# Optimization experiments

Measured on AMD Instinct MI355X. Metric: run time of the kernel, lower is better.

Reference implementation:

```python
import jax, jax.numpy as jnp
import numpy as np


def setup_inputs() -> dict:
    key = jax.random.key(0)
    B, T, V, H, C = 128, 256, 128, 512, 128  # batch, seq_length, input_dim, num_hidden, num_classes
    ks = jax.random.split(key, 10)

    def xavier(k, shape):
        fan_in, fan_out = shape
        lim = jnp.sqrt(6.0 / (fan_in + fan_out)).astype(jnp.float32)
        return jax.random.uniform(k, shape, jnp.float32, -lim, lim)

    inp = {
        'x': jax.random.randint(ks[0], (B, T), 0, V, dtype=jnp.int32),
        'W_xg': xavier(ks[1], (V, H)), 'W_hg': xavier(ks[2], (H, H)),
        'W_xi': xavier(ks[3], (V, H)), 'W_hi': xavier(ks[4], (H, H)),
        'W_xf': xavier(ks[5], (V, H)), 'W_hf': xavier(ks[6], (H, H)),
        'W_xo': xavier(ks[7], (V, H)), 'W_ho': xavier(ks[8], (H, H)),
        'W_hp': xavier(ks[9], (H, C)),
        'b_g': jnp.zeros((H,), jnp.float32), 'b_i': jnp.zeros((H,), jnp.float32),
        'b_f': jnp.zeros((H,), jnp.float32), 'b_o': jnp.zeros((H,), jnp.float32),
        'b_p': jnp.zeros((C,), jnp.float32),
    }
    return inp


def reference(x, W_xg, W_hg, W_xi, W_hi, W_xf, W_hf, W_xo, W_ho, W_hp,
              b_g, b_i, b_f, b_o, b_p):
    B, T = x.shape
    H = W_hg.shape[0]
    # one-hot(x_t) @ W_x* == row-gather W_x*[x_t]; same math, no dense one-hot.
    xs = x[:, : T - 1].T  # [T-1, B] token ids; loop runs seq_length-1 steps

    def step(carry, idx):
        h, c = carry
        g = jnp.tanh(W_xg[idx] + h @ W_hg + b_g)
        i = jax.nn.sigmoid(W_xi[idx] + h @ W_hi + b_i)
        f = jax.nn.sigmoid(W_xf[idx] + h @ W_hf + b_f)
        o = jax.nn.sigmoid(W_xo[idx] + h @ W_ho + b_o)
        c = g * i + c * f
        h = jnp.tanh(c) * o
        return (h, c), None

    h0 = jnp.zeros((B, H), jnp.float32)
    c0 = jnp.zeros((B, H), jnp.float32)
    (h, _), _ = jax.lax.scan(step, (h0, c0), xs)
    return h @ W_hp + b_p
```

## Files before the change

kernel.cpp:

```cpp
#include <hip/hip_runtime.h>


typedef __attribute__((ext_vector_type(8))) short short8;
typedef __attribute__((ext_vector_type(4))) float f32x4;
typedef __attribute__((ext_vector_type(4))) unsigned int u32x4;
typedef __attribute__((ext_vector_type(8))) unsigned int u32x8;
typedef __attribute__((ext_vector_type(16))) unsigned int u32x16;

#define NGROUPS 8
#define WGS_PER_GROUP 32
#define HDIM 512
#define TT 256
#define NSTEPS 255
#define CDIM 128
#define PGQ 4096
#define TAGB_OFF 1024

__device__ unsigned long long g_hbuf[4 * NGROUPS * PGQ];
__device__ unsigned int g_sync[TAGB_OFF + NGROUPS * WGS_PER_GROUP * 16];

static __device__ __forceinline__ unsigned short f32_to_bf16(float f) {
  unsigned int u = __builtin_bit_cast(unsigned int, f);
  u += 0x7fffu + ((u >> 16) & 1u);
  return (unsigned short)(u >> 16);
}
static __device__ __forceinline__ float bf16_to_f32(unsigned short s) {
  unsigned int u = ((unsigned int)s) << 16;
  return __builtin_bit_cast(float, u);
}
static __device__ __forceinline__ float fast_sigmoid(float v) {
  return __builtin_amdgcn_rcpf(1.0f + __expf(-v));
}
static __device__ __forceinline__ float fast_tanh(float v) {
  return 1.0f - 2.0f * __builtin_amdgcn_rcpf(1.0f + __expf(2.0f * v));
}
static __device__ __forceinline__ const unsigned int* sgpr_ptr(const unsigned int* p) {
  const unsigned long long u = (unsigned long long)p;
  const unsigned int lo = __builtin_amdgcn_readfirstlane((unsigned int)u);
  const unsigned int hi = __builtin_amdgcn_readfirstlane((unsigned int)(u >> 32));
  return (const unsigned int*)(((unsigned long long)hi << 32) | (unsigned long long)lo);
}

static __device__ __forceinline__ unsigned int poll_min8(const unsigned int* p) {
  u32x8 A;
  asm volatile("s_dcache_inv\n\t"
               "s_load_dwordx8 %0, %1, 0x0\n\t"
               "s_waitcnt lgkmcnt(0)"
               : "=&s"(A) : "s"(p) : "memory");
  unsigned int m = A[0];
#pragma unroll
  for (int i = 1; i < 8; ++i) m = (A[i] < m) ? A[i] : m;
  return m;
}
static __device__ __forceinline__ unsigned int poll_min32(const unsigned int* p) {
  u32x16 A, B;
  asm volatile("s_dcache_inv\n\t"
               "s_load_dwordx16 %0, %1, 0x0\n\t"
               "s_waitcnt lgkmcnt(0)"
               : "=&s"(A) : "s"(p) : "memory");
  unsigned int m = A[0];
#pragma unroll
  for (int i = 1; i < 16; ++i) m = (A[i] < m) ? A[i] : m;
  asm volatile("s_load_dwordx16 %0, %1, 0x40\n\t"
               "s_waitcnt lgkmcnt(0)"
               : "=&s"(B) : "s"(p) : "memory");
#pragma unroll
  for (int i = 0; i < 16; ++i) m = (B[i] < m) ? B[i] : m;
  return m;
}

static __device__ __forceinline__ void wait_prod8(const unsigned int* tag8,
                                                  const unsigned int* tagBlane,
                                                  unsigned int tgt) {
  for (int spins = 0; spins < 4096; ++spins) {
    if (poll_min8(tag8) >= tgt) return;
  }
  for (;;) {
    const unsigned int v = __hip_atomic_load(tagBlane, __ATOMIC_RELAXED,
                                             __HIP_MEMORY_SCOPE_AGENT);
    if (__all((int)(v >= tgt))) return;
    __builtin_amdgcn_s_sleep(1);
  }
}
static __device__ __forceinline__ void wait_group32(const unsigned int* tagA,
                                                    const unsigned int* tagBlane,
                                                    unsigned int tgt) {
  for (int spins = 0; spins < 4096; ++spins) {
    if (poll_min32(tagA) >= tgt) return;
  }
  for (;;) {
    const unsigned int v = __hip_atomic_load(tagBlane, __ATOMIC_RELAXED,
                                             __HIP_MEMORY_SCOPE_AGENT);
    if (__all((int)(v >= tgt))) return;
    __builtin_amdgcn_s_sleep(1);
  }
}

__global__ __launch_bounds__(256, 1) void lstm_persistent(
    const int* __restrict__ x,
    const float* __restrict__ Wxg, const float* __restrict__ Whg,
    const float* __restrict__ Wxi, const float* __restrict__ Whi,
    const float* __restrict__ Wxf, const float* __restrict__ Whf,
    const float* __restrict__ Wxo, const float* __restrict__ Who,
    const float* __restrict__ Whp,
    const float* __restrict__ bg, const float* __restrict__ bi,
    const float* __restrict__ bf, const float* __restrict__ bo,
    const float* __restrict__ bp,
    float* __restrict__ out)
{
  const int bid = blockIdx.x;
  const int g = bid & 7;
  const int w = bid >> 3;
  const int tid = threadIdx.x;
  const int wave = tid >> 6;
  const int lane = tid & 63;
  const int lane15 = lane & 15;
  const int lanehi = lane >> 4;

  __shared__ float part[2][4][4][16][16];
  __shared__ int lds_x[16][TT];
  __shared__ unsigned int lds_ctr;

  if (tid == 0) lds_ctr = 0u;
  for (int i = tid; i < 16 * TT; i += 256)
    ((int*)lds_x)[i] = x[g * 16 * TT + i];

  const float* Whs[4] = {Whg, Whi, Whf, Who};
  const int bcol = (w << 4) + lane15;
  short8 wf[4][4][2];
#pragma unroll
  for (int gate = 0; gate < 4; ++gate) {
    const float* Wh = Whs[gate];
#pragma unroll
    for (int ksl = 0; ksl < 4; ++ksl) {
      const int ksg = (wave << 2) + ksl;
      short8 s0, s1;
#pragma unroll
      for (int e = 0; e < 8; ++e) {
        float v = Wh[(ksg * 32 + lanehi * 8 + e) * HDIM + bcol];
        unsigned short a = f32_to_bf16(v);
        unsigned short b = f32_to_bf16(v - bf16_to_f32(a));
        s0[e] = (short)a; s1[e] = (short)b;
      }
      wf[gate][ksl][0] = s0; wf[gate][ksl][1] = s1;
    }
  }
  __syncthreads();

  const int brow = tid >> 4;
  const int jl = tid & 15;
  const int j = (w << 4) + jl;
  const float bgv = bg[j], biv = bi[j], bfv = bf[j], bov = bo[j];
  const int pidx = ((j >> 5) << 8) + ((((j >> 3) & 3) << 4) + brow) * 4 + ((j & 7) >> 1);

  const unsigned int* tagA = sgpr_ptr(g_sync + (g << 5));
  const unsigned int* tag8 = sgpr_ptr(g_sync + (g << 5) + (wave << 3));
  const unsigned int* tagBlane =
      g_sync + TAGB_OFF + ((unsigned)(g * 32 + (lane & 31)) << 4);
  unsigned int* myA = g_sync + (g << 5) + w;
  unsigned int* myB = g_sync + TAGB_OFF + ((unsigned)(g * 32 + w) << 4);

  float creg = 0.0f;

  for (int t = 0; t < NSTEPS; ++t) {
    const int idx = lds_x[brow][t];
    const float xgv = Wxg[idx * HDIM + j];
    const float xiv = Wxi[idx * HDIM + j];
    const float xfv = Wxf[idx * HDIM + j];
    const float xov = Wxo[idx * HDIM + j];

    f32x4 acc[4] = {{0.f,0.f,0.f,0.f},{0.f,0.f,0.f,0.f},
                    {0.f,0.f,0.f,0.f},{0.f,0.f,0.f,0.f}};
    if (t > 0) {
      wait_prod8(tag8, tagBlane, (unsigned int)t);
      const unsigned long long* srcq =
          g_hbuf + ((size_t)((t & 3) * NGROUPS + g)) * PGQ;
      unsigned long long q[16];
#pragma unroll
      for (int ksl = 0; ksl < 4; ++ksl) {
        const int base = ((wave << 2) + ksl) * 256 + (lane << 2);
#pragma unroll
        for (int u = 0; u < 4; ++u)
          q[ksl * 4 + u] = srcq[base + u];
      }
#pragma unroll
      for (int ksl = 0; ksl < 4; ++ksl) {
        u32x4 lo, hi;
#pragma unroll
        for (int u = 0; u < 4; ++u) {
          lo[u] = (unsigned int)q[ksl * 4 + u];
          hi[u] = (unsigned int)(q[ksl * 4 + u] >> 32);
        }
        const short8 a0 = __builtin_bit_cast(short8, lo);
        const short8 a1 = __builtin_bit_cast(short8, hi);
#pragma unroll
        for (int gate = 0; gate < 4; ++gate) {
          acc[gate] = __builtin_amdgcn_mfma_f32_16x16x32_bf16(a0, wf[gate][ksl][0], acc[gate], 0, 0, 0);
          acc[gate] = __builtin_amdgcn_mfma_f32_16x16x32_bf16(a0, wf[gate][ksl][1], acc[gate], 0, 0, 0);
          acc[gate] = __builtin_amdgcn_mfma_f32_16x16x32_bf16(a1, wf[gate][ksl][0], acc[gate], 0, 0, 0);
        }
      }
    }
    {
      const int crow = lanehi << 2;
      const int pb = t & 1;
#pragma unroll
      for (int gate = 0; gate < 4; ++gate)
#pragma unroll
        for (int r = 0; r < 4; ++r)
          part[pb][wave][gate][crow + r][lane15] = acc[gate][r];
    }
    __syncthreads();

    const int pb = t & 1;
    const float pg = part[pb][0][0][brow][jl] + part[pb][1][0][brow][jl] +
                     part[pb][2][0][brow][jl] + part[pb][3][0][brow][jl] + xgv + bgv;
    const float pi = part[pb][0][1][brow][jl] + part[pb][1][1][brow][jl] +
                     part[pb][2][1][brow][jl] + part[pb][3][1][brow][jl] + xiv + biv;
    const float pf = part[pb][0][2][brow][jl] + part[pb][1][2][brow][jl] +
                     part[pb][2][2][brow][jl] + part[pb][3][2][brow][jl] + xfv + bfv;
    const float po = part[pb][0][3][brow][jl] + part[pb][1][3][brow][jl] +
                     part[pb][2][3][brow][jl] + part[pb][3][3][brow][jl] + xov + bov;
    const float gv = fast_tanh(pg);
    const float iv = fast_sigmoid(pi);
    const float fv = fast_sigmoid(pf);
    const float ov = fast_sigmoid(po);
    creg = gv * iv + creg * fv;
    const float hv = fast_tanh(creg) * ov;

    const unsigned short h0 = f32_to_bf16(hv);
    const unsigned short h1 = f32_to_bf16(hv - bf16_to_f32(h0));
    const unsigned int pa = (unsigned int)h0 | ((unsigned int)h1 << 16);
    const unsigned int na = (unsigned int)__shfl_xor((int)pa, 1);
    if (!(jl & 1)) {
      unsigned long long* dstq =
          g_hbuf + ((size_t)(((t + 1) & 3) * NGROUPS + g)) * PGQ;
      const unsigned int w0 = (pa & 0xffffu) | ((na & 0xffffu) << 16);
      const unsigned int w1 = (pa >> 16) | (na & 0xffff0000u);
      dstq[pidx] = (unsigned long long)w0 | ((unsigned long long)w1 << 32);
    }
    asm volatile("s_waitcnt vmcnt(0)" ::: "memory");
    if (lane == 0) {
      const unsigned int old = atomicAdd(&lds_ctr, 1u);
      if ((old & 3u) == 3u) {
        __hip_atomic_store(myA, (unsigned int)(t + 1), __ATOMIC_RELAXED,
                           __HIP_MEMORY_SCOPE_WORKGROUP);
        __hip_atomic_store(myB, (unsigned int)(t + 1), __ATOMIC_RELAXED,
                           __HIP_MEMORY_SCOPE_AGENT);
      }
    }
  }

  wait_group32(tagA, tagBlane, (unsigned int)NSTEPS);
  __syncthreads();
  {
    const unsigned long long* srcq =
        g_hbuf + ((size_t)((NSTEPS & 3) * NGROUPS + g)) * PGQ;
    const int bq = tid >> 4;
    const int q15 = tid & 15;
    const int cloc = q15 >> 2;
    const int ksl2 = q15 & 3;
    const int cc = (w << 2) + cloc;
    float sum = 0.0f;
    for (int k = ksl2 * 128; k < ksl2 * 128 + 128; k += 2) {
      const int pk = ((k >> 5) << 8) + ((((k >> 3) & 3) << 4) + bq) * 4 + ((k & 7) >> 1);
      const unsigned long long qv = srcq[pk];
      const unsigned int w0 = (unsigned int)qv;
      const unsigned int w1 = (unsigned int)(qv >> 32);
      const float hk0 = bf16_to_f32((unsigned short)(w0 & 0xffffu)) +
                        bf16_to_f32((unsigned short)(w1 & 0xffffu));
      const float hk1 = bf16_to_f32((unsigned short)(w0 >> 16)) +
                        bf16_to_f32((unsigned short)(w1 >> 16));
      sum += hk0 * Whp[k * CDIM + cc] + hk1 * Whp[(k + 1) * CDIM + cc];
    }
    float* gb = &part[0][0][0][0][0];
    gb[tid] = sum;
    __syncthreads();
    if (ksl2 == 0) {
      const float res = gb[tid] + gb[tid + 1] + gb[tid + 2] + gb[tid + 3] + bp[cc];
      out[(g * 16 + bq) * CDIM + cc] = res;
    }
  }
}

extern "C" void kernel_launch(void* const* d_in, const int* in_sizes, int n_in,
                              void* d_out, int out_size, void* d_ws, size_t ws_size,
                              hipStream_t stream) {
  (void)in_sizes; (void)n_in; (void)out_size; (void)d_ws; (void)ws_size;
  const int* x = (const int*)d_in[0];
  const float* Wxg = (const float*)d_in[1];
  const float* Whg = (const float*)d_in[2];
  const float* Wxi = (const float*)d_in[3];
  const float* Whi = (const float*)d_in[4];
  const float* Wxf = (const float*)d_in[5];
  const float* Whf = (const float*)d_in[6];
  const float* Wxo = (const float*)d_in[7];
  const float* Who = (const float*)d_in[8];
  const float* Whp = (const float*)d_in[9];
  const float* bg = (const float*)d_in[10];
  const float* bi = (const float*)d_in[11];
  const float* bf = (const float*)d_in[12];
  const float* bo = (const float*)d_in[13];
  const float* bp = (const float*)d_in[14];
  float* out = (float*)d_out;

  void* sync_dev = nullptr;
  hipGetSymbolAddress(&sync_dev, HIP_SYMBOL(g_sync));
  hipMemsetAsync(sync_dev, 0,
                 sizeof(unsigned int) * (TAGB_OFF + NGROUPS * WGS_PER_GROUP * 16),
                 stream);

  lstm_persistent<<<dim3(256), dim3(256), 0, stream>>>(
      x, Wxg, Whg, Wxi, Whi, Wxf, Whf, Wxo, Who, Whp,
      bg, bi, bf, bo, bp, out);
}
```

Measured before the change: 417.4 us.

## Split hidden-state buffer into hi/lo planes and vectorize partial-sum LDS layout

The global h exchange buffer changes from interleaved 64-bit hi/lo pairs to two separate 32-bit planes, so each lane loads each MFMA operand with one 16-byte vector load instead of four 64-bit loads followed by unpacking. The MFMA chain is split across two accumulator sets to shorten the dependency chain. The LDS partial-sum layout becomes gate-innermost, so each thread does one float4 store per row and four float4 loads in the reduction. The cost is two scalar stores per producer instead of one 64-bit store.

Measured after the change: 418.1 us. About the same (+0.2%).

```diff
diff --git a/kernel.cpp b/kernel.cpp
--- a/kernel.cpp
+++ b/kernel.cpp
@@ -3,7 +3,6 @@
 
 typedef __attribute__((ext_vector_type(8))) short short8;
 typedef __attribute__((ext_vector_type(4))) float f32x4;
-typedef __attribute__((ext_vector_type(4))) unsigned int u32x4;
 typedef __attribute__((ext_vector_type(8))) unsigned int u32x8;
 typedef __attribute__((ext_vector_type(16))) unsigned int u32x16;
 
@@ -13,10 +12,11 @@
 #define TT 256
 #define NSTEPS 255
 #define CDIM 128
-#define PGQ 4096
+#define PGW 8192
+#define PLANE_W 4096
 #define TAGB_OFF 1024
 
-__device__ unsigned long long g_hbuf[4 * NGROUPS * PGQ];
+__device__ unsigned int g_hbuf[4 * NGROUPS * PGW];
 __device__ unsigned int g_sync[TAGB_OFF + NGROUPS * WGS_PER_GROUP * 16];
 
 static __device__ __forceinline__ unsigned short f32_to_bf16(float f) {
@@ -117,7 +117,7 @@
   const int lane15 = lane & 15;
   const int lanehi = lane >> 4;
 
-  __shared__ float part[2][4][4][16][16];
+  __shared__ __align__(16) float part[2][4][16][16][4];
   __shared__ int lds_x[16][TT];
   __shared__ unsigned int lds_ctr;
 
@@ -151,7 +151,8 @@
   const int jl = tid & 15;
   const int j = (w << 4) + jl;
   const float bgv = bg[j], biv = bi[j], bfv = bf[j], bov = bo[j];
-  const int pidx = ((j >> 5) << 8) + ((((j >> 3) & 3) << 4) + brow) * 4 + ((j & 7) >> 1);
+  const int woff32 = ((j >> 5) << 8) + ((((j >> 3) & 3) << 4) + brow) * 4 + ((j & 7) >> 1);
+  const unsigned int voff = ((unsigned)wave << 12) + ((unsigned)lane << 4);
 
   const unsigned int* tagA = sgpr_ptr(g_sync + (g << 5));
   const unsigned int* tag8 = sgpr_ptr(g_sync + (g << 5) + (wave << 3));
@@ -169,35 +170,36 @@
     const float xfv = Wxf[idx * HDIM + j];
     const float xov = Wxo[idx * HDIM + j];
 
-    f32x4 acc[4] = {{0.f,0.f,0.f,0.f},{0.f,0.f,0.f,0.f},
-                    {0.f,0.f,0.f,0.f},{0.f,0.f,0.f,0.f}};
+    f32x4 accA[4] = {{0.f,0.f,0.f,0.f},{0.f,0.f,0.f,0.f},
+                     {0.f,0.f,0.f,0.f},{0.f,0.f,0.f,0.f}};
+    f32x4 accB[4] = {{0.f,0.f,0.f,0.f},{0.f,0.f,0.f,0.f},
+                     {0.f,0.f,0.f,0.f},{0.f,0.f,0.f,0.f}};
     if (t > 0) {
       wait_prod8(tag8, tagBlane, (unsigned int)t);
-      const unsigned long long* srcq =
-          g_hbuf + ((size_t)((t & 3) * NGROUPS + g)) * PGQ;
-      unsigned long long q[16];
+      const char* p0 = (const char*)(g_hbuf +
+          ((size_t)((t & 3) * NGROUPS + g)) * PGW) + voff;
+      short8 a0[4], a1[4];
 #pragma unroll
       for (int ksl = 0; ksl < 4; ++ksl) {
-        const int base = ((wave << 2) + ksl) * 256 + (lane << 2);
-#pragma unroll
-        for (int u = 0; u < 4; ++u)
-          q[ksl * 4 + u] = srcq[base + u];
-      }
-#pragma unroll
-      for (int ksl = 0; ksl < 4; ++ksl) {
-        u32x4 lo, hi;
-#pragma unroll
-        for (int u = 0; u < 4; ++u) {
-          lo[u] = (unsigned int)q[ksl * 4 + u];
-          hi[u] = (unsigned int)(q[ksl * 4 + u] >> 32);
+        a0[ksl] = *(const short8*)(p0 + ksl * 1024);
+        a1[ksl] = *(const short8*)(p0 + PLANE_W * 4 + ksl * 1024);
+      }
+#pragma unroll
+      for (int ksl = 0; ksl < 2; ++ksl) {
+#pragma unroll
+        for (int gate = 0; gate < 4; ++gate) {
+          accA[gate] = __builtin_amdgcn_mfma_f32_16x16x32_bf16(a0[ksl], wf[gate][ksl][0], accA[gate], 0, 0, 0);
+          accA[gate] = __builtin_amdgcn_mfma_f32_16x16x32_bf16(a0[ksl], wf[gate][ksl][1], accA[gate], 0, 0, 0);
+          accA[gate] = __builtin_amdgcn_mfma_f32_16x16x32_bf16(a1[ksl], wf[gate][ksl][0], accA[gate], 0, 0, 0);
         }
-        const short8 a0 = __builtin_bit_cast(short8, lo);
-        const short8 a1 = __builtin_bit_cast(short8, hi);
+      }
+#pragma unroll
+      for (int ksl = 2; ksl < 4; ++ksl) {
 #pragma unroll
         for (int gate = 0; gate < 4; ++gate) {
-          acc[gate] = __builtin_amdgcn_mfma_f32_16x16x32_bf16(a0, wf[gate][ksl][0], acc[gate], 0, 0, 0);
-          acc[gate] = __builtin_amdgcn_mfma_f32_16x16x32_bf16(a0, wf[gate][ksl][1], acc[gate], 0, 0, 0);
-          acc[gate] = __builtin_amdgcn_mfma_f32_16x16x32_bf16(a1, wf[gate][ksl][0], acc[gate], 0, 0, 0);
+          accB[gate] = __builtin_amdgcn_mfma_f32_16x16x32_bf16(a0[ksl], wf[gate][ksl][0], accB[gate], 0, 0, 0);
+          accB[gate] = __builtin_amdgcn_mfma_f32_16x16x32_bf16(a0[ksl], wf[gate][ksl][1], accB[gate], 0, 0, 0);
+          accB[gate] = __builtin_amdgcn_mfma_f32_16x16x32_bf16(a1[ksl], wf[gate][ksl][0], accB[gate], 0, 0, 0);
         }
       }
     }
@@ -205,22 +207,26 @@
       const int crow = lanehi << 2;
       const int pb = t & 1;
 #pragma unroll
-      for (int gate = 0; gate < 4; ++gate)
-#pragma unroll
-        for (int r = 0; r < 4; ++r)
-          part[pb][wave][gate][crow + r][lane15] = acc[gate][r];
+      for (int r = 0; r < 4; ++r) {
+        f32x4 vr;
+#pragma unroll
+        for (int gate = 0; gate < 4; ++gate)
+          vr[gate] = accA[gate][r] + accB[gate][r];
+        *(f32x4*)&part[pb][wave][crow + r][lane15][0] = vr;
+      }
     }
     __syncthreads();
 
     const int pb = t & 1;
-    const float pg = part[pb][0][0][brow][jl] + part[pb][1][0][brow][jl] +
-                     part[pb][2][0][brow][jl] + part[pb][3][0][brow][jl] + xgv + bgv;
-    const float pi = part[pb][0][1][brow][jl] + part[pb][1][1][brow][jl] +
-                     part[pb][2][1][brow][jl] + part[pb][3][1][brow][jl] + xiv + biv;
-    const float pf = part[pb][0][2][brow][jl] + part[pb][1][2][brow][jl] +
-                     part[pb][2][2][brow][jl] + part[pb][3][2][brow][jl] + xfv + bfv;
-    const float po = part[pb][0][3][brow][jl] + part[pb][1][3][brow][jl] +
-                     part[pb][2][3][brow][jl] + part[pb][3][3][brow][jl] + xov + bov;
+    const f32x4 s0 = *(const f32x4*)&part[pb][0][brow][jl][0];
+    const f32x4 s1 = *(const f32x4*)&part[pb][1][brow][jl][0];
+    const f32x4 s2 = *(const f32x4*)&part[pb][2][brow][jl][0];
+    const f32x4 s3 = *(const f32x4*)&part[pb][3][brow][jl][0];
+    const f32x4 pre = s0 + s1 + s2 + s3;
+    const float pg = pre[0] + xgv + bgv;
+    const float pi = pre[1] + xiv + biv;
+    const float pf = pre[2] + xfv + bfv;
+    const float po = pre[3] + xov + bov;
     const float gv = fast_tanh(pg);
     const float iv = fast_sigmoid(pi);
     const float fv = fast_sigmoid(pf);
@@ -233,11 +239,12 @@
     const unsigned int pa = (unsigned int)h0 | ((unsigned int)h1 << 16);
     const unsigned int na = (unsigned int)__shfl_xor((int)pa, 1);
     if (!(jl & 1)) {
-      unsigned long long* dstq =
-          g_hbuf + ((size_t)(((t + 1) & 3) * NGROUPS + g)) * PGQ;
+      unsigned int* dst0 = g_hbuf +
+          ((size_t)(((t + 1) & 3) * NGROUPS + g)) * PGW;
       const unsigned int w0 = (pa & 0xffffu) | ((na & 0xffffu) << 16);
       const unsigned int w1 = (pa >> 16) | (na & 0xffff0000u);
-      dstq[pidx] = (unsigned long long)w0 | ((unsigned long long)w1 << 32);
+      dst0[woff32] = w0;
+      dst0[PLANE_W + woff32] = w1;
     }
     asm volatile("s_waitcnt vmcnt(0)" ::: "memory");
     if (lane == 0) {
@@ -254,8 +261,8 @@
   wait_group32(tagA, tagBlane, (unsigned int)NSTEPS);
   __syncthreads();
   {
-    const unsigned long long* srcq =
-        g_hbuf + ((size_t)((NSTEPS & 3) * NGROUPS + g)) * PGQ;
+    const unsigned int* src =
+        g_hbuf + ((size_t)((NSTEPS & 3) * NGROUPS + g)) * PGW;
     const int bq = tid >> 4;
     const int q15 = tid & 15;
     const int cloc = q15 >> 2;
@@ -264,9 +271,8 @@
     float sum = 0.0f;
     for (int k = ksl2 * 128; k < ksl2 * 128 + 128; k += 2) {
       const int pk = ((k >> 5) << 8) + ((((k >> 3) & 3) << 4) + bq) * 4 + ((k & 7) >> 1);
-      const unsigned long long qv = srcq[pk];
-      const unsigned int w0 = (unsigned int)qv;
-      const unsigned int w1 = (unsigned int)(qv >> 32);
+      const unsigned int w0 = src[pk];
+      const unsigned int w1 = src[PLANE_W + pk];
       const float hk0 = bf16_to_f32((unsigned short)(w0 & 0xffffu)) +
                         bf16_to_f32((unsigned short)(w1 & 0xffffu));
       const float hk1 = bf16_to_f32((unsigned short)(w0 >> 16)) +
```
